# Kernel optimization log

Hardware: AMD Instinct MI355X
Metric: run time of the kernel (lower is better)

The kernel has to match this reference:

```python
import jax, jax.numpy as jnp
import numpy as np

ALPHA = 1.0
BETA = 10.0
MARGIN = 0.5


def setup_inputs() -> dict:
    key = jax.random.key(0)
    k1, k2 = jax.random.split(key)
    emb = jax.random.normal(k1, (4096, 512), dtype=jnp.float32)
    # module docstring: embeddings are L2-normalized
    emb = emb / jnp.linalg.norm(emb, axis=1, keepdims=True)
    labels = jax.random.randint(k2, (4096,), 0, 64, dtype=jnp.int64)
    return {"embeddings": emb, "labels": labels}


def reference(embeddings, labels):
    n = embeddings.shape[0]
    sim = embeddings @ embeddings.T  # [n, n]
    labels_eq = labels[None, :] == labels[:, None]
    eye = jnp.eye(n, dtype=bool)
    pos_mask = labels_eq & ~eye
    neg_mask = ~labels_eq & ~eye

    # masked exp-sums (masked entries contribute 0, matching torch's
    # clone/NEG_INF/zero-out dance without materializing extra copies)
    pos_exp = jnp.where(pos_mask, jnp.exp(-ALPHA * (sim - MARGIN)), 0.0)
    neg_exp = jnp.where(neg_mask, jnp.exp(BETA * (sim - MARGIN)), 0.0)
    pos_term = (1.0 / ALPHA) * jnp.log1p(pos_exp.sum(axis=1))
    neg_term = (1.0 / BETA) * jnp.log1p(neg_exp.sum(axis=1))

    valid = pos_mask.any(axis=1) & neg_mask.any(axis=1)
    n_valid = valid.sum()
    total = jnp.where(valid, pos_term + neg_term, 0.0).sum()
    return jnp.where(n_valid > 0, total / jnp.maximum(n_valid, 1).astype(sim.dtype), 0.0)
```

## Files before the change

### kernel.cpp

```cpp
#include <hip/hip_runtime.h>
#include <hip/hip_bf16.h>

#define N 4096
#define D 512
#define MARGIN 0.5f
#define BETA 10.0f
#define NT (D / 32)
#define NBLOCKS 528

typedef __attribute__((ext_vector_type(8))) short short8;
typedef __attribute__((ext_vector_type(4))) float floatx4;

__device__ inline unsigned short f2bf(float f) {
    unsigned u = __float_as_uint(f);
    u += 0x7fffu + ((u >> 16) & 1u);
    return (unsigned short)(u >> 16);
}

__global__ __launch_bounds__(256) void convert_bf16_kernel(
        const float4* __restrict__ in, ushort4* __restrict__ out,
        float* __restrict__ sums ) {
    int idx = blockIdx.x * 256 + threadIdx.x;
    if (idx < 2 * N) sums[idx] = 0.f;
    float4 v = in[idx];
    ushort4 o;
    o.x = f2bf(v.x); o.y = f2bf(v.y); o.z = f2bf(v.z); o.w = f2bf(v.w);
    out[idx] = o;
}

__global__ __launch_bounds__(256, 2) void ms_loss_gemm(
        const unsigned short* __restrict__ Ebf,
        const int* __restrict__ labels,
        float* __restrict__ pos_sum,
        float* __restrict__ neg_sum) {
    __shared__ unsigned short slab[4][2][2][64 * 32];
    __shared__ int rlab[128];
    __shared__ int clab[128];

    int t = blockIdx.x;
    int bi = 0;
    while (t >= (32 - bi)) { t -= (32 - bi); ++bi; }
    const int bj = bi + t;
    const bool diag = (bi == bj);

    const int tid  = threadIdx.x;
    const int wave = tid >> 6;
    const int lane = tid & 63;
    const int quad = lane >> 4;
    const int lcol = lane & 15;
    const int wrow = wave >> 1;
    const int wcol = wave & 1;
    const int ibase = bi * 128;
    const int jbase = bj * 128;

    if (tid < 128)       rlab[tid]       = labels[ibase + tid];
    else                 clab[tid - 128] = labels[jbase + tid - 128];

    floatx4 acc[4][4];
#pragma unroll
    for (int mt = 0; mt < 4; ++mt)
#pragma unroll
        for (int nt = 0; nt < 4; ++nt)
            acc[mt][nt] = (floatx4){0.f, 0.f, 0.f, 0.f};

    const char* Eb = (const char*)Ebf;
    char* myBase = (char*)&slab[wave][0][0][0];
    const int arow = ibase + wrow * 64;
    const int brow = jbase + wcol * 64;
    const int srow = lane >> 2;
    const int sckb = ((lane & 3) ^ ((lane >> 3) & 3)) * 16;
    const int rdsw = ((lcol >> 1) & 3);

#define STAGE(BUF, KT)                                                         \
    do {                                                                       \
        const int kb_ = (KT) * 64;                                             \
        char* la_ = myBase + (BUF) * 8192;                                     \
        _Pragma("unroll")                                                      \
        for (int it_ = 0; it_ < 4; ++it_) {                                    \
            int r_  = it_ * 16 + srow;                                         \
            int lo_ = it_ * 1024 + lane * 16;                                  \
            const char* ga_ = Eb + (size_t)(arow + r_) * (D * 2) + kb_ + sckb; \
            __builtin_amdgcn_global_load_lds(                                  \
                (const __attribute__((address_space(1))) void*)ga_,            \
                (__attribute__((address_space(3))) void*)(la_ + lo_), 16, 0, 0);\
            const char* gb_ = Eb + (size_t)(brow + r_) * (D * 2) + kb_ + sckb; \
            __builtin_amdgcn_global_load_lds(                                  \
                (const __attribute__((address_space(1))) void*)gb_,            \
                (__attribute__((address_space(3))) void*)(la_ + 4096 + lo_), 16, 0, 0);\
        }                                                                      \
    } while (0)

#define COMPUTE(CUR)                                                           \
    do {                                                                       \
        const char* Ar = myBase + (CUR) * 8192;                                \
        const char* Br = Ar + 4096;                                            \
        short8 a[4], b[4];                                                     \
        const int rchunk = (quad ^ rdsw) * 16;                                 \
        _Pragma("unroll")                                                      \
        for (int mt = 0; mt < 4; ++mt) {                                       \
            int r = mt * 16 + lcol;                        \
            a[mt] = *(const short8*)(Ar + r * 64 + rchunk);                    \
        }                                                                      \
        _Pragma("unroll")                                                      \
        for (int nt = 0; nt < 4; ++nt) {                                       \
            int c = nt * 16 + lcol;                        \
            b[nt] = *(const short8*)(Br + c * 64 + rchunk);                    \
        }                                                                      \
        _Pragma("unroll")                                                      \
        for (int mt = 0; mt < 4; ++mt)                                         \
            _Pragma("unroll")                                                  \
            for (int nt = 0; nt < 4; ++nt)                                     \
                acc[mt][nt] = __builtin_amdgcn_mfma_f32_16x16x32_bf16(         \
                    a[mt], b[nt], acc[mt][nt], 0, 0, 0);                       \
    } while (0)

    STAGE(0, 0);

    for (int kt = 0; kt < NT - 1; ++kt) {
        STAGE((kt + 1) & 1, kt + 1);
        asm volatile("s_waitcnt vmcnt(8)" ::: "memory");
        __builtin_amdgcn_sched_barrier(0);
        COMPUTE(kt & 1);
    }
    asm volatile("s_waitcnt vmcnt(0)" ::: "memory");
    __builtin_amdgcn_sched_barrier(0);
    COMPUTE((NT - 1) & 1);

#undef STAGE
#undef COMPUTE

    __syncthreads();

    int ljv[4], gjv[4];
#pragma unroll
    for (int nt = 0; nt < 4; ++nt) {
        int cl = wcol * 64 + nt * 16 + lcol;
        ljv[nt] = clab[cl];
        gjv[nt] = jbase + cl;
    }

    float colp[4] = {0.f, 0.f, 0.f, 0.f};
    float coln[4] = {0.f, 0.f, 0.f, 0.f};

#pragma unroll
    for (int mt = 0; mt < 4; ++mt) {
#pragma unroll
        for (int reg = 0; reg < 4; ++reg) {
            int rl = wrow * 64 + mt * 16 + quad * 4 + reg;
            int gi = ibase + rl;
            int li = rlab[rl];
            float p = 0.f, ng = 0.f;
#pragma unroll
            for (int nt = 0; nt < 4; ++nt) {
                float s = acc[mt][nt][reg];
                if (gi != gjv[nt]) {
                    if (li == ljv[nt]) {
                        float e = __expf(MARGIN - s);
                        p += e;  colp[nt] += e;
                    } else {
                        float e = __expf(BETA * (s - MARGIN));
                        ng += e; coln[nt] += e;
                    }
                }
            }
            p  += __shfl_xor(p, 1);   ng += __shfl_xor(ng, 1);
            p  += __shfl_xor(p, 2);   ng += __shfl_xor(ng, 2);
            p  += __shfl_xor(p, 4);   ng += __shfl_xor(ng, 4);
            p  += __shfl_xor(p, 8);   ng += __shfl_xor(ng, 8);
            if (lcol == 0) {
                atomicAdd(&pos_sum[gi], p);
                atomicAdd(&neg_sum[gi], ng);
            }
        }
    }

    if (!diag) {
#pragma unroll
        for (int nt = 0; nt < 4; ++nt) {
            float cp = colp[nt], cn = coln[nt];
            cp += __shfl_xor(cp, 16);  cn += __shfl_xor(cn, 16);
            cp += __shfl_xor(cp, 32);  cn += __shfl_xor(cn, 32);
            if (quad == 0) {
                int gj = gjv[nt];
                atomicAdd(&pos_sum[gj], cp);
                atomicAdd(&neg_sum[gj], cn);
            }
        }
    }
}

__global__ __launch_bounds__(1024) void finalize_kernel(
        const float4* __restrict__ pos4, const float4* __restrict__ neg4,
        float* __restrict__ out) {
    __shared__ float sb[16];
    __shared__ int   sc[16];
    const int tid = threadIdx.x;
    float4 p  = pos4[tid];
    float4 ng = neg4[tid];
    const float* pp = (const float*)&p;
    const float* nn = (const float*)&ng;
    float tot = 0.f;
    int cnt = 0;
#pragma unroll
    for (int j = 0; j < 4; ++j) {
        if (pp[j] > 0.f && nn[j] > 0.f) {
            tot += log1pf(pp[j]) + (1.0f / BETA) * log1pf(nn[j]);
            cnt += 1;
        }
    }
#pragma unroll
    for (int s = 1; s < 64; s <<= 1) {
        tot += __shfl_xor(tot, s);
        cnt += __shfl_xor(cnt, s);
    }
    if ((tid & 63) == 0) { sb[tid >> 6] = tot; sc[tid >> 6] = cnt; }
    __syncthreads();
    if (tid < 16) {
        float t2 = sb[tid];
        int   c2 = sc[tid];
#pragma unroll
        for (int s = 1; s < 16; s <<= 1) {
            t2 += __shfl_xor(t2, s);
            c2 += __shfl_xor(c2, s);
        }
        if (tid == 0) out[0] = (c2 > 0) ? t2 / (float)c2 : 0.f;
    }
}

extern "C" void kernel_launch(void* const* d_in, const int* in_sizes, int n_in,
                              void* d_out, int out_size, void* d_ws, size_t ws_size,
                              hipStream_t stream) {
    const float* emb   = (const float*)d_in[0];
    const int* labels  = (const int*)d_in[1];
    float* out         = (float*)d_out;

    char* ws = (char*)d_ws;
    unsigned short* Ebf = (unsigned short*)ws;
    float* pos_sum = (float*)(ws + (size_t)N * D * 2);
    float* neg_sum = pos_sum + N;

    convert_bf16_kernel<<<(N * D / 4) / 256, 256, 0, stream>>>(
        (const float4*)emb, (ushort4*)Ebf, pos_sum);

    ms_loss_gemm<<<NBLOCKS, 256, 0, stream>>>(Ebf, labels, pos_sum, neg_sum);

    finalize_kernel<<<1, 1024, 0, stream>>>(
        (const float4*)pos_sum, (const float4*)neg_sum, out);
}
```

Baseline: 98.58 us.

## Load MFMA fragments directly from global memory into registers, dropping LDS staging

Replaces the per-wave async global-to-LDS staging, with its swizzled layout and LDS fragment reads, by direct global loads of the bf16 fragments into registers. A register double buffer (a0/b0, a1/b1) lets the next k-step's loads overlap the current MFMAs. This removes LDS traffic and the explicit waitcnt barriers, at the cost of more VGPRs and of relying on compiler scheduling and L1/L2 hits for latency hiding. Each lane's 16-byte loads are strided by whole rows, so coalescing per instruction is worse.

Measured after the change: 118.3 us. +20.0%, slower.

```diff
diff --git a/kernel.cpp b/kernel.cpp
--- a/kernel.cpp
+++ b/kernel.cpp
@@ -33,7 +33,6 @@
         const int* __restrict__ labels,
         float* __restrict__ pos_sum,
         float* __restrict__ neg_sum) {
-    __shared__ unsigned short slab[4][2][2][64 * 32];
     __shared__ int rlab[128];
     __shared__ int clab[128];
 
@@ -64,70 +63,40 @@
             acc[mt][nt] = (floatx4){0.f, 0.f, 0.f, 0.f};
 
     const char* Eb = (const char*)Ebf;
-    char* myBase = (char*)&slab[wave][0][0][0];
-    const int arow = ibase + wrow * 64;
-    const int brow = jbase + wcol * 64;
-    const int srow = lane >> 2;
-    const int sckb = ((lane & 3) ^ ((lane >> 3) & 3)) * 16;
-    const int rdsw = ((lcol >> 1) & 3);
-
-#define STAGE(BUF, KT)                                                         \
+    const char* pa = Eb + (size_t)(ibase + wrow * 64 + lcol) * 1024 + quad * 16;
+    const char* pb = Eb + (size_t)(jbase + wcol * 64 + lcol) * 1024 + quad * 16;
+
+#define LOADF(A, B, KT)                                                        \
     do {                                                                       \
-        const int kb_ = (KT) * 64;                                             \
-        char* la_ = myBase + (BUF) * 8192;                                     \
+        const int ko_ = (KT) * 64;                                             \
         _Pragma("unroll")                                                      \
-        for (int it_ = 0; it_ < 4; ++it_) {                                    \
-            int r_  = it_ * 16 + srow;                                         \
-            int lo_ = it_ * 1024 + lane * 16;                                  \
-            const char* ga_ = Eb + (size_t)(arow + r_) * (D * 2) + kb_ + sckb; \
-            __builtin_amdgcn_global_load_lds(                                  \
-                (const __attribute__((address_space(1))) void*)ga_,            \
-                (__attribute__((address_space(3))) void*)(la_ + lo_), 16, 0, 0);\
-            const char* gb_ = Eb + (size_t)(brow + r_) * (D * 2) + kb_ + sckb; \
-            __builtin_amdgcn_global_load_lds(                                  \
-                (const __attribute__((address_space(1))) void*)gb_,            \
-                (__attribute__((address_space(3))) void*)(la_ + 4096 + lo_), 16, 0, 0);\
-        }                                                                      \
+        for (int mt = 0; mt < 4; ++mt)                                         \
+            (A)[mt] = *(const short8*)(pa + mt * 16384 + ko_);                 \
+        _Pragma("unroll")                                                      \
+        for (int nt = 0; nt < 4; ++nt)                                         \
+            (B)[nt] = *(const short8*)(pb + nt * 16384 + ko_);                 \
     } while (0)
 
-#define COMPUTE(CUR)                                                           \
+#define MFMAC(A, B)                                                            \
     do {                                                                       \
-        const char* Ar = myBase + (CUR) * 8192;                                \
-        const char* Br = Ar + 4096;                                            \
-        short8 a[4], b[4];                                                     \
-        const int rchunk = (quad ^ rdsw) * 16;                                 \
-        _Pragma("unroll")                                                      \
-        for (int mt = 0; mt < 4; ++mt) {                                       \
-            int r = mt * 16 + lcol;                        \
-            a[mt] = *(const short8*)(Ar + r * 64 + rchunk);                    \
-        }                                                                      \
-        _Pragma("unroll")                                                      \
-        for (int nt = 0; nt < 4; ++nt) {                                       \
-            int c = nt * 16 + lcol;                        \
-            b[nt] = *(const short8*)(Br + c * 64 + rchunk);                    \
-        }                                                                      \
         _Pragma("unroll")                                                      \
         for (int mt = 0; mt < 4; ++mt)                                         \
             _Pragma("unroll")                                                  \
             for (int nt = 0; nt < 4; ++nt)                                     \
                 acc[mt][nt] = __builtin_amdgcn_mfma_f32_16x16x32_bf16(         \
-                    a[mt], b[nt], acc[mt][nt], 0, 0, 0);                       \
+                    (A)[mt], (B)[nt], acc[mt][nt], 0, 0, 0);                   \
     } while (0)
 
-    STAGE(0, 0);
-
-    for (int kt = 0; kt < NT - 1; ++kt) {
-        STAGE((kt + 1) & 1, kt + 1);
-        asm volatile("s_waitcnt vmcnt(8)" ::: "memory");
-        __builtin_amdgcn_sched_barrier(0);
-        COMPUTE(kt & 1);
-    }
-    asm volatile("s_waitcnt vmcnt(0)" ::: "memory");
-    __builtin_amdgcn_sched_barrier(0);
-    COMPUTE((NT - 1) & 1);
-
-#undef STAGE
-#undef COMPUTE
+    short8 a0[4], b0[4], a1[4], b1[4];
+    LOADF(a0, b0, 0);
+    for (int i = 0; i < NT / 2; ++i) {
+        LOADF(a1, b1, 2 * i + 1);
+        MFMAC(a0, b0);
+        if (i < NT / 2 - 1) LOADF(a0, b0, 2 * i + 2);
+        MFMAC(a1, b1);
+    }
+#undef LOADF
+#undef MFMAC
 
     __syncthreads();
 
```
